# Performance work log

Hardware: AMD Instinct MI355X
Metric: run time of the kernel (lower is better)

## Reference

```python
import jax, jax.numpy as jnp
import numpy as np

N_NODES = 50000
N_EDGES = 800000
IN_DIM = 128
HIDDEN = 128
NUM_CLASSES = 64
NEG_SLOPE = 0.2


def setup_inputs() -> dict:
    key = jax.random.key(0)
    ks = jax.random.split(key, 12)
    x = jax.random.normal(ks[0], (N_NODES, IN_DIM), dtype=jnp.float32)
    src = jax.random.randint(ks[1], (N_EDGES,), 0, N_NODES, dtype=jnp.int64)
    dst = jax.random.randint(ks[2], (N_EDGES,), 0, N_NODES, dtype=jnp.int64)
    def glorot(k, shape):
        fan_in, fan_out = shape[0], shape[-1]
        s = jnp.sqrt(2.0 / (fan_in + fan_out)).astype(jnp.float32)
        return jax.random.normal(k, shape, dtype=jnp.float32) * s
    return {
        "x": x, "src": src, "dst": dst,
        # GATConv params (1 head, no bias, no residual)
        "W_gat": glorot(ks[3], (IN_DIM, HIDDEN)),
        "attn_l": glorot(ks[4], (HIDDEN,)),
        "attn_r": glorot(ks[5], (HIDDEN,)),
        # GraphConv params (norm='none', bias=True)
        "W1": glorot(ks[6], (HIDDEN, HIDDEN)),
        "b1": jnp.zeros((HIDDEN,), dtype=jnp.float32),
        "W2": glorot(ks[7], (HIDDEN, HIDDEN)),
        "b2": jnp.zeros((HIDDEN,), dtype=jnp.float32),
        "Wc": glorot(ks[8], (HIDDEN, NUM_CLASSES)),
        "bc": jnp.zeros((NUM_CLASSES,), dtype=jnp.float32),
    }


def reference(x, src, dst, W_gat, attn_l, attn_r, W1, b1, W2, b2, Wc, bc):
    N = x.shape[0]
    # --- GATConv, single head, eval mode (dropout=0) ---
    h = x @ W_gat                      # (N, H)
    el = h @ attn_l                    # (N,)
    er = h @ attn_r                    # (N,)
    e = jax.nn.leaky_relu(el[src] + er[dst], negative_slope=NEG_SLOPE)  # (E,)
    # edge softmax over incoming edges of each dst node
    emax = jax.ops.segment_max(e, dst, num_segments=N)
    ee = jnp.exp(e - emax[dst])
    esum = jax.ops.segment_sum(ee, dst, num_segments=N)
    alpha = ee / esum[dst]             # (E,) attention = reused edge weights
    h1 = jax.ops.segment_sum(h[src] * alpha[:, None], dst, num_segments=N)
    h1 = jax.nn.elu(h1)                # GATConv activation

    # --- GraphConv (norm='none') with edge_weight = alpha ---
    def gconv(hin, W, b):
        hp = hin @ W                                   # project (order is math-equivalent)
        agg = jax.ops.segment_sum(hp[src] * alpha[:, None], dst, num_segments=N)
        return agg + b

    h2 = gconv(h1, W1, b1)
    h3 = gconv(h2, W2, b2)
    logits = gconv(h3, Wc, bc)         # (N, num_classes)
    return logits
```

## Files before the change

kernel.cpp:

```cpp
#include <hip/hip_runtime.h>
#include <hip/hip_fp16.h>
#include <math.h>

#define N_NODES 50000
#define N_EDGES 800000
#define PAD_EDGES (N_EDGES + 8 * N_NODES)

typedef _Float16 half8 __attribute__((ext_vector_type(8)));
typedef float floatx16 __attribute__((ext_vector_type(16)));

__global__ __launch_bounds__(256) void prep_k(const float* __restrict__ Wg,
                                              __half* __restrict__ out) {
  int e = blockIdx.x * 256 + threadIdx.x;
  if (e >= 16384) return;
  _Float16* o = (_Float16*)out;
  int k = e >> 7, n = e & 127;
  float w = Wg[k * 128 + n];
  _Float16 hi = (_Float16)w;
  float lo = w - (float)hi;
  int oi = (((k >> 3) * 128 + n) << 3) | (k & 7);
  o[oi] = hi;
  o[16384 + oi] = (_Float16)lo;
}

__global__ __launch_bounds__(256) void prep12_k(const float* __restrict__ W1,
                                                const float* __restrict__ W2,
                                                const float* __restrict__ b1,
                                                float* __restrict__ W12,
                                                float* __restrict__ c12) {
  int e = blockIdx.x * 256 + threadIdx.x;
  if (e < 16384) {
    int k = e >> 7, n = e & 127;
    float acc = 0.f;
    for (int j = 0; j < 128; ++j) acc = fmaf(W1[k * 128 + j], W2[j * 128 + n], acc);
    W12[k * 128 + n] = acc;
  } else if (e < 16512) {
    int n = e - 16384;
    float acc = 0.f;
    for (int j = 0; j < 128; ++j) acc = fmaf(b1[j], W2[j * 128 + n], acc);
    c12[n] = acc;
  }
}

__global__ __launch_bounds__(256) void prepP_k(const float* __restrict__ W12,
                                               const float* __restrict__ c12,
                                               const float* __restrict__ Wc,
                                               const float* __restrict__ b2,
                                               __half* __restrict__ WPhl,
                                               float* __restrict__ c1,
                                               float* __restrict__ c2) {
  int e = blockIdx.x * 256 + threadIdx.x;
  _Float16* o = (_Float16*)WPhl;
  if (e < 8192) {
    int k = e >> 6, n = e & 63;
    float acc = 0.f;
    for (int j = 0; j < 128; ++j) acc = fmaf(W12[k * 128 + j], Wc[j * 64 + n], acc);
    _Float16 hi = (_Float16)acc;
    float lo = acc - (float)hi;
    int oi = (((k >> 3) * 64 + n) << 3) | (k & 7);
    o[oi] = hi;
    o[8192 + oi] = (_Float16)lo;
  } else if (e < 8256) {
    int n = e - 8192;
    float acc = 0.f;
    for (int j = 0; j < 128; ++j) acc = fmaf(c12[j], Wc[j * 64 + n], acc);
    c1[n] = acc;
  } else if (e < 8320) {
    int n = e - 8256;
    float acc = 0.f;
    for (int j = 0; j < 128; ++j) acc = fmaf(b2[j], Wc[j * 64 + n], acc);
    c2[n] = acc;
  }
}

template <int NCOL, bool A16, bool ELR>
__global__ __launch_bounds__(256) void mgemm_k(const void* __restrict__ Ap,
                                               const __half* __restrict__ Whl,
                                               __half* __restrict__ C16, int M,
                                               const float* __restrict__ al,
                                               const float* __restrict__ ar,
                                               float* __restrict__ el,
                                               float* __restrict__ er) {
  __shared__ __half Al[16][129][8];
  const int tid  = threadIdx.x;
  const int row0 = blockIdx.x * 128;
  const int lane = tid & 63;
  const int lane31 = lane & 31;
  const int q = lane >> 5;
  const int r = tid >> 6;

  if (A16) {
    const uint4* A8 = (const uint4*)Ap;
    #pragma unroll
    for (int i = 0; i < 8; ++i) {
      int idx = tid + i * 256;
      int row = idx >> 4, c = idx & 15;
      int grow = row0 + row;
      uint4 v = make_uint4(0u, 0u, 0u, 0u);
      if (grow < M) v = A8[grow * 16 + c];
      *reinterpret_cast<uint4*>(&Al[c][row][0]) = v;
    }
  } else {
    const float4* A4 = (const float4*)Ap;
    #pragma unroll
    for (int i = 0; i < 8; ++i) {
      int idx = tid + i * 256;
      int row = idx >> 4, c = idx & 15;
      int grow = row0 + row;
      half8 hv = {};
      if (grow < M) {
        float4 a0 = A4[grow * 32 + c * 2];
        float4 a1 = A4[grow * 32 + c * 2 + 1];
        hv[0] = (_Float16)a0.x; hv[1] = (_Float16)a0.y;
        hv[2] = (_Float16)a0.z; hv[3] = (_Float16)a0.w;
        hv[4] = (_Float16)a1.x; hv[5] = (_Float16)a1.y;
        hv[6] = (_Float16)a1.z; hv[7] = (_Float16)a1.w;
      }
      *reinterpret_cast<half8*>(&Al[c][row][0]) = hv;
    }
  }
  __syncthreads();

  half8 afr[8];
  #pragma unroll
  for (int s = 0; s < 8; ++s)
    afr[s] = *reinterpret_cast<const half8*>(&Al[2 * s + q][r * 32 + lane31][0]);

  const half8* B8 = reinterpret_cast<const half8*>(Whl);
  const int KN8 = 16 * NCOL;

  float elp[16], erp[16];
  if (ELR) {
    #pragma unroll
    for (int i = 0; i < 16; ++i) { elp[i] = 0.f; erp[i] = 0.f; }
  }

  #pragma unroll
  for (int tc = 0; tc < NCOL / 32; ++tc) {
    floatx16 acc = {};
    int nbase = tc * 32 + lane31;
    #pragma unroll
    for (int s = 0; s < 8; ++s) {
      int ci = (2 * s + q) * NCOL + nbase;
      half8 bl = B8[KN8 + ci];
      half8 bh = B8[ci];
      acc = __builtin_amdgcn_mfma_f32_32x32x16_f16(afr[s], bl, acc, 0, 0, 0);
      acc = __builtin_amdgcn_mfma_f32_32x32x16_f16(afr[s], bh, acc, 0, 0, 0);
    }
    if (ELR) {
      float alv = al[nbase], arv = ar[nbase];
      #pragma unroll
      for (int i = 0; i < 16; ++i) {
        elp[i] = fmaf(acc[i], alv, elp[i]);
        erp[i] = fmaf(acc[i], arv, erp[i]);
      }
    }
    #pragma unroll
    for (int i = 0; i < 16; ++i) {
      int rl = (i & 3) + 8 * (i >> 2) + 4 * q;
      int grow = row0 + r * 32 + rl;
      if (grow < M) C16[grow * NCOL + nbase] = __float2half(acc[i]);
    }
  }

  if (ELR) {
    #pragma unroll
    for (int off = 1; off <= 16; off <<= 1) {
      #pragma unroll
      for (int i = 0; i < 16; ++i) {
        elp[i] += __shfl_xor(elp[i], off);
        erp[i] += __shfl_xor(erp[i], off);
      }
    }
    if (lane31 == 0) {
      #pragma unroll
      for (int i = 0; i < 16; ++i) {
        int rl = (i & 3) + 8 * (i >> 2) + 4 * q;
        int grow = row0 + r * 32 + rl;
        if (grow < M) { el[grow] = elp[i]; er[grow] = erp[i]; }
      }
    }
  }
}

__global__ __launch_bounds__(256) void hist_k(const int* __restrict__ dst,
                                              int* __restrict__ deg,
                                              int* __restrict__ rank, int E) {
  int e = blockIdx.x * 256 + threadIdx.x;
  if (e < E) rank[e] = atomicAdd(&deg[dst[e]], 1);
}

__global__ __launch_bounds__(256) void scan1_k(const int* __restrict__ deg,
                                               int* __restrict__ offs,
                                               int* __restrict__ bsum, int N) {
  __shared__ int s[256];
  int t = threadIdx.x;
  int i = blockIdx.x * 256 + t;
  int v = 0;
  if (i < N) {
    int d = deg[i];
    v = (d + 7) & ~7;
    if (v < 8) v = 8;
  }
  s[t] = v;
  __syncthreads();
  for (int o = 1; o < 256; o <<= 1) {
    int add = (t >= o) ? s[t - o] : 0;
    __syncthreads();
    s[t] += add;
    __syncthreads();
  }
  if (i < N) offs[i] = s[t] - v;
  if (t == 255) bsum[blockIdx.x] = s[255];
}

__global__ __launch_bounds__(256) void scan2_k(int* __restrict__ bsum, int nb) {
  __shared__ int s[256];
  int t = threadIdx.x;
  int v = (t < nb) ? bsum[t] : 0;
  s[t] = v;
  __syncthreads();
  for (int o = 1; o < 256; o <<= 1) {
    int add = (t >= o) ? s[t - o] : 0;
    __syncthreads();
    s[t] += add;
    __syncthreads();
  }
  if (t < nb) bsum[t] = s[t] - v;
}

__global__ __launch_bounds__(256) void scan3_k(int* __restrict__ offs,
                                               const int* __restrict__ deg,
                                               const int* __restrict__ bsum, int N) {
  int i = blockIdx.x * 256 + threadIdx.x;
  if (i < N) {
    int o = offs[i] + bsum[blockIdx.x];
    offs[i] = o;
    if (i == N - 1) {
      int d = deg[i];
      int pd = (d + 7) & ~7;
      if (pd < 8) pd = 8;
      offs[N] = o + pd;
    }
  }
}

__global__ __launch_bounds__(256) void scatter_k(const int* __restrict__ src,
                                                 const int* __restrict__ dst,
                                                 const int* __restrict__ offs,
                                                 const int* __restrict__ rank,
                                                 int* __restrict__ csr_src, int E) {
  int e = blockIdx.x * 256 + threadIdx.x;
  if (e < E) {
    csr_src[offs[dst[e]] + rank[e]] = src[e];
  }
}

__device__ inline void fma8(float2 acc[4], uint4 u, float a) {
  __half2* h = reinterpret_cast<__half2*>(&u);
  #pragma unroll
  for (int j = 0; j < 4; ++j) {
    float2 f = __half22float2(h[j]);
    acc[j].x = fmaf(a, f.x, acc[j].x);
    acc[j].y = fmaf(a, f.y, acc[j].y);
  }
}

__global__ __launch_bounds__(256) void aggsm_k(const int* __restrict__ offs,
                                               const int* __restrict__ deg,
                                               const int* __restrict__ csr_src,
                                               const float* __restrict__ el,
                                               const float* __restrict__ er,
                                               int2* __restrict__ meta,
                                               float* __restrict__ t,
                                               const __half* __restrict__ hp,
                                               __half* __restrict__ out, int N) {
  int w    = (blockIdx.x * 256 + threadIdx.x) >> 6;
  int lane = threadIdx.x & 63;
  if (w >= N) return;
  int o0   = offs[w];
  int pcnt = offs[w + 1] - o0;
  int cnt  = deg[w];
  int q   = lane >> 4;
  int fl  = lane & 15;
  const uint4* hpq = reinterpret_cast<const uint4*>(hp);

  int   myS = 0;
  float myA = 0.f;

  if (cnt <= 64) {
    bool valid = lane < cnt;
    float erv = er[w];
    int s = 0;
    float ev = -3.4e38f;
    if (valid) {
      s = csr_src[o0 + lane];
      float e0 = el[s] + erv;
      ev = (e0 >= 0.f) ? e0 : 0.2f * e0;
    }
    float m = ev;
    #pragma unroll
    for (int off = 32; off; off >>= 1) m = fmaxf(m, __shfl_xor(m, off));
    float ee = valid ? __expf(ev - m) : 0.f;
    float sum = ee;
    #pragma unroll
    for (int off = 32; off; off >>= 1) sum += __shfl_xor(sum, off);
    float tp = 0.f;
    if (valid) {
      float a = ee / sum;
      meta[o0 + lane] = make_int2(s * 16, __float_as_int(a));
      myS = s; myA = a;
      tp = (deg[s] > 0) ? a : 0.f;
    } else if (lane < pcnt) {
      meta[o0 + lane] = make_int2(0, 0);
    }
    #pragma unroll
    for (int off = 32; off; off >>= 1) tp += __shfl_xor(tp, off);
    if (lane == 0) t[w] = tp;
  } else {
    float erv = er[w];
    float m = -3.4e38f;
    for (int i = lane; i < cnt; i += 64) {
      int s = csr_src[o0 + i];
      float ev = el[s] + erv;
      ev = (ev >= 0.f) ? ev : 0.2f * ev;
      m = fmaxf(m, ev);
    }
    #pragma unroll
    for (int off = 32; off; off >>= 1) m = fmaxf(m, __shfl_xor(m, off));
    float sum = 0.f, tacc = 0.f;
    for (int i = lane; i < cnt; i += 64) {
      int s = csr_src[o0 + i];
      float ev = el[s] + erv;
      ev = (ev >= 0.f) ? ev : 0.2f * ev;
      float ee = __expf(ev - m);
      meta[o0 + i] = make_int2(s * 16, __float_as_int(ee));
      sum += ee;
      tacc += (deg[s] > 0) ? ee : 0.f;
    }
    #pragma unroll
    for (int off = 32; off; off >>= 1) {
      sum += __shfl_xor(sum, off);
      tacc += __shfl_xor(tacc, off);
    }
    float inv = 1.f / sum;
    if (lane == 0) t[w] = tacc * inv;
    for (int i = lane; i < cnt; i += 64) {
      int2 mm = meta[o0 + i];
      meta[o0 + i] = make_int2(mm.x, __float_as_int(__int_as_float(mm.y) * inv));
    }
    for (int i = cnt + lane; i < pcnt; i += 64) meta[o0 + i] = make_int2(0, 0);
    if (lane < cnt) {
      int2 mm = meta[o0 + lane];
      myS = mm.x >> 4; myA = __int_as_float(mm.y);
    }
  }

  float2 acc0[4] = {}, acc1[4] = {}, acc2[4] = {}, acc3[4] = {};
  int cntc = cnt < 64 ? cnt : 64;
  if (cntc > 0) {
    int cr = (cntc + 15) & ~15;
    int   sA = __shfl(myS, q),          sB = __shfl(myS, 4 + q);
    int   sC = __shfl(myS, 8 + q),      sD = __shfl(myS, 12 + q);
    float aA = __shfl(myA, q),          aB = __shfl(myA, 4 + q);
    float aC = __shfl(myA, 8 + q),      aD = __shfl(myA, 12 + q);
    uint4 vA = hpq[sA * 16 + fl], vB = hpq[sB * 16 + fl];
    uint4 vC = hpq[sC * 16 + fl], vD = hpq[sD * 16 + fl];
    for (int base = 16; base < cr; base += 16) {
      int   tA = __shfl(myS, base + q),      tB = __shfl(myS, base + 4 + q);
      int   tC = __shfl(myS, base + 8 + q),  tD = __shfl(myS, base + 12 + q);
      float nA = __shfl(myA, base + q),      nB = __shfl(myA, base + 4 + q);
      float nC = __shfl(myA, base + 8 + q),  nD = __shfl(myA, base + 12 + q);
      uint4 wA = hpq[tA * 16 + fl], wB = hpq[tB * 16 + fl];
      uint4 wC = hpq[tC * 16 + fl], wD = hpq[tD * 16 + fl];
      fma8(acc0, vA, aA);
      fma8(acc1, vB, aB);
      fma8(acc2, vC, aC);
      fma8(acc3, vD, aD);
      vA = wA; vB = wB; vC = wC; vD = wD;
      aA = nA; aB = nB; aC = nC; aD = nD;
    }
    fma8(acc0, vA, aA);
    fma8(acc1, vB, aB);
    fma8(acc2, vC, aC);
    fma8(acc3, vD, aD);
  }
  for (int p = o0 + 64 + q; p < o0 + cnt; p += 4) {
    int2 mm = meta[p];
    fma8(acc0, hpq[mm.x + fl], __int_as_float(mm.y));
  }
  #pragma unroll
  for (int j = 0; j < 4; ++j) {
    acc0[j].x += acc1[j].x + acc2[j].x + acc3[j].x;
    acc0[j].y += acc1[j].y + acc2[j].y + acc3[j].y;
  }
  #pragma unroll
  for (int off = 16; off <= 32; off <<= 1) {
    #pragma unroll
    for (int j = 0; j < 4; ++j) {
      acc0[j].x += __shfl_xor(acc0[j].x, off);
      acc0[j].y += __shfl_xor(acc0[j].y, off);
    }
  }
  if (q == 0) {
    float o8[8];
    #pragma unroll
    for (int j = 0; j < 4; ++j) { o8[2 * j] = acc0[j].x; o8[2 * j + 1] = acc0[j].y; }
    #pragma unroll
    for (int j = 0; j < 8; ++j) o8[j] = (o8[j] > 0.f) ? o8[j] : (__expf(o8[j]) - 1.f);
    __half2 p0 = __floats2half2_rn(o8[0], o8[1]);
    __half2 p1 = __floats2half2_rn(o8[2], o8[3]);
    __half2 p2 = __floats2half2_rn(o8[4], o8[5]);
    __half2 p3 = __floats2half2_rn(o8[6], o8[7]);
    uint4 pk;
    pk.x = *reinterpret_cast<unsigned*>(&p0);
    pk.y = *reinterpret_cast<unsigned*>(&p1);
    pk.z = *reinterpret_cast<unsigned*>(&p2);
    pk.w = *reinterpret_cast<unsigned*>(&p3);
    *reinterpret_cast<uint4*>(&out[w * 128 + fl * 8]) = pk;
  }
}

template <bool FINAL>
__global__ __launch_bounds__(256) void agg64v_k(const int* __restrict__ offs,
                                                const int2* __restrict__ meta,
                                                const __half* __restrict__ zp,
                                                const float* __restrict__ t,
                                                const int* __restrict__ deg,
                                                const float* __restrict__ c1,
                                                const float* __restrict__ c2,
                                                const float* __restrict__ bc,
                                                void* __restrict__ outp, int N) {
  int w    = (blockIdx.x * 256 + threadIdx.x) >> 6;
  int lane = threadIdx.x & 63;
  if (w >= N) return;
  int o0 = offs[w], o1 = offs[w + 1];
  int o   = lane >> 3;
  int fl  = lane & 7;
  const uint4* hpq = reinterpret_cast<const uint4*>(zp);

  float2 acc0[4] = {};
  int p = o0 + o;
  int2 mA = meta[p];
  for (; p + 8 < o1; p += 8) {
    int2 nA = meta[p + 8];
    uint4 vA = hpq[(mA.x >> 1) + fl];
    fma8(acc0, vA, __int_as_float(mA.y));
    mA = nA;
  }
  {
    uint4 vA = hpq[(mA.x >> 1) + fl];
    fma8(acc0, vA, __int_as_float(mA.y));
  }
  #pragma unroll
  for (int off = 8; off <= 32; off <<= 1) {
    #pragma unroll
    for (int j = 0; j < 4; ++j) {
      acc0[j].x += __shfl_xor(acc0[j].x, off);
      acc0[j].y += __shfl_xor(acc0[j].y, off);
    }
  }
  if (o == 0) {
    float o8[8];
    #pragma unroll
    for (int j = 0; j < 4; ++j) { o8[2 * j] = acc0[j].x; o8[2 * j + 1] = acc0[j].y; }
    if (FINAL) {
      float tw = t[w];
      float dw = (deg[w] > 0) ? 1.f : 0.f;
      float4 a0 = reinterpret_cast<const float4*>(c1)[fl * 2];
      float4 a1 = reinterpret_cast<const float4*>(c1)[fl * 2 + 1];
      float4 d0 = reinterpret_cast<const float4*>(c2)[fl * 2];
      float4 d1 = reinterpret_cast<const float4*>(c2)[fl * 2 + 1];
      float4 b0 = reinterpret_cast<const float4*>(bc)[fl * 2];
      float4 b1v = reinterpret_cast<const float4*>(bc)[fl * 2 + 1];
      o8[0] += tw * a0.x + dw * d0.x + b0.x;
      o8[1] += tw * a0.y + dw * d0.y + b0.y;
      o8[2] += tw * a0.z + dw * d0.z + b0.z;
      o8[3] += tw * a0.w + dw * d0.w + b0.w;
      o8[4] += tw * a1.x + dw * d1.x + b1v.x;
      o8[5] += tw * a1.y + dw * d1.y + b1v.y;
      o8[6] += tw * a1.z + dw * d1.z + b1v.z;
      o8[7] += tw * a1.w + dw * d1.w + b1v.w;
      float4* of = reinterpret_cast<float4*>(outp);
      of[w * 16 + fl * 2]     = make_float4(o8[0], o8[1], o8[2], o8[3]);
      of[w * 16 + fl * 2 + 1] = make_float4(o8[4], o8[5], o8[6], o8[7]);
    } else {
      __half2 p0 = __floats2half2_rn(o8[0], o8[1]);
      __half2 p1 = __floats2half2_rn(o8[2], o8[3]);
      __half2 p2 = __floats2half2_rn(o8[4], o8[5]);
      __half2 p3 = __floats2half2_rn(o8[6], o8[7]);
      uint4 pk;
      pk.x = *reinterpret_cast<unsigned*>(&p0);
      pk.y = *reinterpret_cast<unsigned*>(&p1);
      pk.z = *reinterpret_cast<unsigned*>(&p2);
      pk.w = *reinterpret_cast<unsigned*>(&p3);
      reinterpret_cast<uint4*>(outp)[w * 8 + fl] = pk;
    }
  }
}

extern "C" void kernel_launch(void* const* d_in, const int* in_sizes, int n_in,
                              void* d_out, int out_size, void* d_ws, size_t ws_size,
                              hipStream_t stream) {
  const float* x      = (const float*)d_in[0];
  const int*   src    = (const int*)d_in[1];
  const int*   dst    = (const int*)d_in[2];
  const float* W_gat  = (const float*)d_in[3];
  const float* attn_l = (const float*)d_in[4];
  const float* attn_r = (const float*)d_in[5];
  const float* W1     = (const float*)d_in[6];
  const float* b1     = (const float*)d_in[7];
  const float* W2     = (const float*)d_in[8];
  const float* b2     = (const float*)d_in[9];
  const float* Wc     = (const float*)d_in[10];
  const float* bc     = (const float*)d_in[11];
  float* out = (float*)d_out;

  char* ws = (char*)d_ws;
  size_t off = 0;
  auto walloc = [&](size_t bytes) -> void* {
    void* p = ws + off;
    off += (bytes + 255) & ~size_t(255);
    return p;
  };
  __half* P16     = (__half*)walloc((size_t)N_NODES * 128 * 2);
  __half* F16     = (__half*)walloc((size_t)N_NODES * 128 * 2);
  float*  el      = (float*)walloc((size_t)N_NODES * 4);
  float*  er      = (float*)walloc((size_t)N_NODES * 4);
  float*  tbuf    = (float*)walloc((size_t)N_NODES * 4);
  int*    deg     = (int*)walloc((size_t)N_NODES * 4);
  int*    offs    = (int*)walloc((size_t)(N_NODES + 1) * 4);
  int*    rank    = (int*)walloc((size_t)N_EDGES * 4);
  int*    csr_src = (int*)walloc((size_t)PAD_EDGES * 4);
  int2*   meta    = (int2*)walloc((size_t)PAD_EDGES * 8);
  int*    bsum    = (int*)walloc(1024);
  __half* Wg_hl   = (__half*)walloc((size_t)32768 * 2);
  __half* WP_hl   = (__half*)walloc((size_t)16384 * 2);
  float*  W12     = (float*)walloc((size_t)16384 * 4);
  float*  c12     = (float*)walloc((size_t)128 * 4);
  float*  c1      = (float*)walloc((size_t)64 * 4);
  float*  c2      = (float*)walloc((size_t)64 * 4);

  hipMemsetAsync(deg, 0, (size_t)N_NODES * 4, stream);

  const dim3 blk(256);
  const int nwave_blocks = (N_NODES + 3) / 4;
  const int nedge_blocks = (N_EDGES + 255) / 256;
  const int nscan_blocks = (N_NODES + 255) / 256;
  const int ngemm_blocks = (N_NODES + 127) / 128;

  prep_k<<<dim3(64), blk, 0, stream>>>(W_gat, Wg_hl);
  prep12_k<<<dim3(65), blk, 0, stream>>>(W1, W2, b1, W12, c12);
  prepP_k<<<dim3(33), blk, 0, stream>>>(W12, c12, Wc, b2, WP_hl, c1, c2);

  mgemm_k<128, false, true><<<dim3(ngemm_blocks), blk, 0, stream>>>(
      x, Wg_hl, P16, N_NODES, attn_l, attn_r, el, er);

  hist_k<<<dim3(nedge_blocks), blk, 0, stream>>>(dst, deg, rank, N_EDGES);
  scan1_k<<<dim3(nscan_blocks), blk, 0, stream>>>(deg, offs, bsum, N_NODES);
  scan2_k<<<dim3(1), blk, 0, stream>>>(bsum, nscan_blocks);
  scan3_k<<<dim3(nscan_blocks), blk, 0, stream>>>(offs, deg, bsum, N_NODES);
  scatter_k<<<dim3(nedge_blocks), blk, 0, stream>>>(src, dst, offs, rank, csr_src, N_EDGES);

  aggsm_k<<<dim3(nwave_blocks), blk, 0, stream>>>(offs, deg, csr_src, el, er, meta, tbuf, P16, F16, N_NODES);
  mgemm_k<64, true, false><<<dim3(ngemm_blocks), blk, 0, stream>>>(
      F16, WP_hl, P16, N_NODES, nullptr, nullptr, nullptr, nullptr);
  agg64v_k<false><<<dim3(nwave_blocks), blk, 0, stream>>>(offs, meta, P16, nullptr, nullptr, nullptr, nullptr, nullptr, F16, N_NODES);
  agg64v_k<false><<<dim3(nwave_blocks), blk, 0, stream>>>(offs, meta, F16, nullptr, nullptr, nullptr, nullptr, nullptr, P16, N_NODES);
  agg64v_k<true><<<dim3(nwave_blocks), blk, 0, stream>>>(offs, meta, P16, tbuf, deg, c1, c2, bc, out, N_NODES);
}
```

Measured before the change: 298.1 us.

## Merge prep kernels, pack el with degree flag, stage aggsm meta in LDS

Fuses the two weight-prep kernels into a single launch. scan3 now writes a packed float2 of el and a has-degree flag, so aggsm reads one value per source instead of separate el and deg gathers. In aggsm the per-edge (src, alpha) pairs are placed in shared memory, replacing the shuffle-based broadcast. The gather loop is also restructured to two accumulators over padded count in steps of 8. This removes one launch, a dependent random gather, and shuffle overhead, at the cost of an extra el2 buffer, a little more scan3 work, and less memory-level parallelism in the gather loop.

```diff
diff --git a/kernel.cpp b/kernel.cpp
--- a/kernel.cpp
+++ b/kernel.cpp
@@ -9,33 +9,31 @@
 typedef _Float16 half8 __attribute__((ext_vector_type(8)));
 typedef float floatx16 __attribute__((ext_vector_type(16)));
 
-__global__ __launch_bounds__(256) void prep_k(const float* __restrict__ Wg,
-                                              __half* __restrict__ out) {
-  int e = blockIdx.x * 256 + threadIdx.x;
-  if (e >= 16384) return;
-  _Float16* o = (_Float16*)out;
-  int k = e >> 7, n = e & 127;
-  float w = Wg[k * 128 + n];
-  _Float16 hi = (_Float16)w;
-  float lo = w - (float)hi;
-  int oi = (((k >> 3) * 128 + n) << 3) | (k & 7);
-  o[oi] = hi;
-  o[16384 + oi] = (_Float16)lo;
-}
-
-__global__ __launch_bounds__(256) void prep12_k(const float* __restrict__ W1,
+__global__ __launch_bounds__(256) void prep_a_k(const float* __restrict__ Wg,
+                                                const float* __restrict__ W1,
                                                 const float* __restrict__ W2,
                                                 const float* __restrict__ b1,
+                                                __half* __restrict__ Wg_hl,
                                                 float* __restrict__ W12,
                                                 float* __restrict__ c12) {
   int e = blockIdx.x * 256 + threadIdx.x;
   if (e < 16384) {
+    _Float16* o = (_Float16*)Wg_hl;
     int k = e >> 7, n = e & 127;
+    float w = Wg[k * 128 + n];
+    _Float16 hi = (_Float16)w;
+    float lo = w - (float)hi;
+    int oi = (((k >> 3) * 128 + n) << 3) | (k & 7);
+    o[oi] = hi;
+    o[16384 + oi] = (_Float16)lo;
+  } else if (e < 32768) {
+    int local = e - 16384;
+    int k = local >> 7, n = local & 127;
     float acc = 0.f;
     for (int j = 0; j < 128; ++j) acc = fmaf(W1[k * 128 + j], W2[j * 128 + n], acc);
     W12[k * 128 + n] = acc;
-  } else if (e < 16512) {
-    int n = e - 16384;
+  } else if (e < 32896) {
+    int n = e - 32768;
     float acc = 0.f;
     for (int j = 0; j < 128; ++j) acc = fmaf(b1[j], W2[j * 128 + n], acc);
     c12[n] = acc;
@@ -231,13 +229,16 @@
 
 __global__ __launch_bounds__(256) void scan3_k(int* __restrict__ offs,
                                                const int* __restrict__ deg,
-                                               const int* __restrict__ bsum, int N) {
+                                               const int* __restrict__ bsum,
+                                               const float* __restrict__ el,
+                                               float2* __restrict__ el2, int N) {
   int i = blockIdx.x * 256 + threadIdx.x;
   if (i < N) {
     int o = offs[i] + bsum[blockIdx.x];
     offs[i] = o;
+    int d = deg[i];
+    el2[i] = make_float2(el[i], (d > 0) ? 1.f : 0.f);
     if (i == N - 1) {
-      int d = deg[i];
       int pd = (d + 7) & ~7;
       if (pd < 8) pd = 8;
       offs[N] = o + pd;
@@ -269,78 +270,80 @@
 __global__ __launch_bounds__(256) void aggsm_k(const int* __restrict__ offs,
                                                const int* __restrict__ deg,
                                                const int* __restrict__ csr_src,
-                                               const float* __restrict__ el,
+                                               const float2* __restrict__ el2,
                                                const float* __restrict__ er,
                                                int2* __restrict__ meta,
                                                float* __restrict__ t,
                                                const __half* __restrict__ hp,
                                                __half* __restrict__ out, int N) {
+  __shared__ int2 lmeta[4][64];
+  int wv   = threadIdx.x >> 6;
   int w    = (blockIdx.x * 256 + threadIdx.x) >> 6;
   int lane = threadIdx.x & 63;
   if (w >= N) return;
   int o0   = offs[w];
   int pcnt = offs[w + 1] - o0;
   int cnt  = deg[w];
-  int q   = lane >> 4;
-  int fl  = lane & 15;
+  int q  = lane >> 4;
+  int fl = lane & 15;
   const uint4* hpq = reinterpret_cast<const uint4*>(hp);
-
-  int   myS = 0;
-  float myA = 0.f;
 
   if (cnt <= 64) {
     bool valid = lane < cnt;
     float erv = er[w];
     int s = 0;
-    float ev = -3.4e38f;
+    float ev = -3.4e38f, flag = 0.f;
     if (valid) {
       s = csr_src[o0 + lane];
-      float e0 = el[s] + erv;
+      float2 e2 = el2[s];
+      float e0 = e2.x + erv;
       ev = (e0 >= 0.f) ? e0 : 0.2f * e0;
+      flag = e2.y;
     }
     float m = ev;
     #pragma unroll
     for (int off = 32; off; off >>= 1) m = fmaxf(m, __shfl_xor(m, off));
     float ee = valid ? __expf(ev - m) : 0.f;
-    float sum = ee;
-    #pragma unroll
-    for (int off = 32; off; off >>= 1) sum += __shfl_xor(sum, off);
-    float tp = 0.f;
-    if (valid) {
-      float a = ee / sum;
-      meta[o0 + lane] = make_int2(s * 16, __float_as_int(a));
-      myS = s; myA = a;
-      tp = (deg[s] > 0) ? a : 0.f;
-    } else if (lane < pcnt) {
-      meta[o0 + lane] = make_int2(0, 0);
-    }
-    #pragma unroll
-    for (int off = 32; off; off >>= 1) tp += __shfl_xor(tp, off);
-    if (lane == 0) t[w] = tp;
+    float sum = ee, tp = ee * flag;
+    #pragma unroll
+    for (int off = 32; off; off >>= 1) {
+      sum += __shfl_xor(sum, off);
+      tp  += __shfl_xor(tp, off);
+    }
+    float inv = (cnt > 0) ? 1.f / sum : 0.f;
+    int2 mm = make_int2(0, 0);
+    if (valid) mm = make_int2(s * 16, __float_as_int(ee * inv));
+    if (lane < pcnt) meta[o0 + lane] = mm;
+    lmeta[wv][lane] = mm;
+    if (lane == 0) t[w] = tp * inv;
   } else {
     float erv = er[w];
     float m = -3.4e38f;
     for (int i = lane; i < cnt; i += 64) {
       int s = csr_src[o0 + i];
-      float ev = el[s] + erv;
+      float2 e2 = el2[s];
+      float ev = e2.x + erv;
       ev = (ev >= 0.f) ? ev : 0.2f * ev;
       m = fmaxf(m, ev);
     }
     #pragma unroll
     for (int off = 32; off; off >>= 1) m = fmaxf(m, __shfl_xor(m, off));
     float sum = 0.f, tacc = 0.f;
+    int myS = 0; float myE = 0.f;
     for (int i = lane; i < cnt; i += 64) {
       int s = csr_src[o0 + i];
-      float ev = el[s] + erv;
+      float2 e2 = el2[s];
+      float ev = e2.x + erv;
       ev = (ev >= 0.f) ? ev : 0.2f * ev;
       float ee = __expf(ev - m);
       meta[o0 + i] = make_int2(s * 16, __float_as_int(ee));
       sum += ee;
-      tacc += (deg[s] > 0) ? ee : 0.f;
+      tacc += ee * e2.y;
+      if (i == lane) { myS = s; myE = ee; }
     }
     #pragma unroll
     for (int off = 32; off; off >>= 1) {
-      sum += __shfl_xor(sum, off);
+      sum  += __shfl_xor(sum, off);
       tacc += __shfl_xor(tacc, off);
     }
     float inv = 1.f / sum;
@@ -350,50 +353,30 @@
       meta[o0 + i] = make_int2(mm.x, __float_as_int(__int_as_float(mm.y) * inv));
     }
     for (int i = cnt + lane; i < pcnt; i += 64) meta[o0 + i] = make_int2(0, 0);
-    if (lane < cnt) {
-      int2 mm = meta[o0 + lane];
-      myS = mm.x >> 4; myA = __int_as_float(mm.y);
-    }
-  }
-
-  float2 acc0[4] = {}, acc1[4] = {}, acc2[4] = {}, acc3[4] = {};
-  int cntc = cnt < 64 ? cnt : 64;
-  if (cntc > 0) {
-    int cr = (cntc + 15) & ~15;
-    int   sA = __shfl(myS, q),          sB = __shfl(myS, 4 + q);
-    int   sC = __shfl(myS, 8 + q),      sD = __shfl(myS, 12 + q);
-    float aA = __shfl(myA, q),          aB = __shfl(myA, 4 + q);
-    float aC = __shfl(myA, 8 + q),      aD = __shfl(myA, 12 + q);
-    uint4 vA = hpq[sA * 16 + fl], vB = hpq[sB * 16 + fl];
-    uint4 vC = hpq[sC * 16 + fl], vD = hpq[sD * 16 + fl];
-    for (int base = 16; base < cr; base += 16) {
-      int   tA = __shfl(myS, base + q),      tB = __shfl(myS, base + 4 + q);
-      int   tC = __shfl(myS, base + 8 + q),  tD = __shfl(myS, base + 12 + q);
-      float nA = __shfl(myA, base + q),      nB = __shfl(myA, base + 4 + q);
-      float nC = __shfl(myA, base + 8 + q),  nD = __shfl(myA, base + 12 + q);
-      uint4 wA = hpq[tA * 16 + fl], wB = hpq[tB * 16 + fl];
-      uint4 wC = hpq[tC * 16 + fl], wD = hpq[tD * 16 + fl];
-      fma8(acc0, vA, aA);
-      fma8(acc1, vB, aB);
-      fma8(acc2, vC, aC);
-      fma8(acc3, vD, aD);
-      vA = wA; vB = wB; vC = wC; vD = wD;
-      aA = nA; aB = nB; aC = nC; aD = nD;
-    }
-    fma8(acc0, vA, aA);
-    fma8(acc1, vB, aB);
-    fma8(acc2, vC, aC);
-    fma8(acc3, vD, aD);
-  }
-  for (int p = o0 + 64 + q; p < o0 + cnt; p += 4) {
+    lmeta[wv][lane] = make_int2(myS * 16, __float_as_int(myE * inv));
+  }
+
+  float2 acc0[4] = {}, acc1[4] = {};
+  int pc = pcnt < 64 ? pcnt : 64;
+  int2 mA = lmeta[wv][q], mB = lmeta[wv][4 + q];
+  for (int base = 8; base < pc; base += 8) {
+    int2 nA = lmeta[wv][base + q], nB = lmeta[wv][base + 4 + q];
+    uint4 vA = hpq[mA.x + fl], vB = hpq[mB.x + fl];
+    fma8(acc0, vA, __int_as_float(mA.y));
+    fma8(acc1, vB, __int_as_float(mB.y));
+    mA = nA; mB = nB;
+  }
+  {
+    uint4 vA = hpq[mA.x + fl], vB = hpq[mB.x + fl];
+    fma8(acc0, vA, __int_as_float(mA.y));
+    fma8(acc1, vB, __int_as_float(mB.y));
+  }
+  for (int p = o0 + 64 + q; p < o0 + pcnt; p += 4) {
     int2 mm = meta[p];
     fma8(acc0, hpq[mm.x + fl], __int_as_float(mm.y));
   }
   #pragma unroll
-  for (int j = 0; j < 4; ++j) {
-    acc0[j].x += acc1[j].x + acc2[j].x + acc3[j].x;
-    acc0[j].y += acc1[j].y + acc2[j].y + acc3[j].y;
-  }
+  for (int j = 0; j < 4; ++j) { acc0[j].x += acc1[j].x; acc0[j].y += acc1[j].y; }
   #pragma unroll
   for (int off = 16; off <= 32; off <<= 1) {
     #pragma unroll
@@ -527,6 +510,7 @@
   __half* F16     = (__half*)walloc((size_t)N_NODES * 128 * 2);
   float*  el      = (float*)walloc((size_t)N_NODES * 4);
   float*  er      = (float*)walloc((size_t)N_NODES * 4);
+  float2* el2     = (float2*)walloc((size_t)N_NODES * 8);
   float*  tbuf    = (float*)walloc((size_t)N_NODES * 4);
   int*    deg     = (int*)walloc((size_t)N_NODES * 4);
   int*    offs    = (int*)walloc((size_t)(N_NODES + 1) * 4);
@@ -549,8 +533,7 @@
   const int nscan_blocks = (N_NODES + 255) / 256;
   const int ngemm_blocks = (N_NODES + 127) / 128;
 
-  prep_k<<<dim3(64), blk, 0, stream>>>(W_gat, Wg_hl);
-  prep12_k<<<dim3(65), blk, 0, stream>>>(W1, W2, b1, W12, c12);
+  prep_a_k<<<dim3(129), blk, 0, stream>>>(W_gat, W1, W2, b1, Wg_hl, W12, c12);
   prepP_k<<<dim3(33), blk, 0, stream>>>(W12, c12, Wc, b2, WP_hl, c1, c2);
 
   mgemm_k<128, false, true><<<dim3(ngemm_blocks), blk, 0, stream>>>(
@@ -559,10 +542,10 @@
   hist_k<<<dim3(nedge_blocks), blk, 0, stream>>>(dst, deg, rank, N_EDGES);
   scan1_k<<<dim3(nscan_blocks), blk, 0, stream>>>(deg, offs, bsum, N_NODES);
   scan2_k<<<dim3(1), blk, 0, stream>>>(bsum, nscan_blocks);
-  scan3_k<<<dim3(nscan_blocks), blk, 0, stream>>>(offs, deg, bsum, N_NODES);
+  scan3_k<<<dim3(nscan_blocks), blk, 0, stream>>>(offs, deg, bsum, el, el2, N_NODES);
   scatter_k<<<dim3(nedge_blocks), blk, 0, stream>>>(src, dst, offs, rank, csr_src, N_EDGES);
 
-  aggsm_k<<<dim3(nwave_blocks), blk, 0, stream>>>(offs, deg, csr_src, el, er, meta, tbuf, P16, F16, N_NODES);
+  aggsm_k<<<dim3(nwave_blocks), blk, 0, stream>>>(offs, deg, csr_src, el2, er, meta, tbuf, P16, F16, N_NODES);
   mgemm_k<64, true, false><<<dim3(ngemm_blocks), blk, 0, stream>>>(
       F16, WP_hl, P16, N_NODES, nullptr, nullptr, nullptr, nullptr);
   agg64v_k<false><<<dim3(nwave_blocks), blk, 0, stream>>>(offs, meta, P16, nullptr, nullptr, nullptr, nullptr, nullptr, F16, N_NODES);
```

Result: faster. 284.0 us (-4.7%).
